# Performance work log

Measured on AMD Instinct MI355X. Metric: run time of the kernel, lower is better.

Reference implementation:

```python
import jax, jax.numpy as jnp
import numpy as np
from jax import lax

# Geometry constants (stand-in for beijing* globals)
A = 96           # beijingAngleNum
P = 4            # beijingPlanes
DET0, DET1 = 256, 8   # beijingSubDetectorSize [u, v]
NZ, NY, NX = 32, 256, 256  # beijingVolumeSize (nz = P * DET1)
T = 256          # ray integration steps
LAMB = 0.01


def _bilinear(vol, ix, iy):
    # vol: [nz, ny, nx]; ix, iy: [...] index-space coords. Zero outside.
    nz, ny, nx = vol.shape
    x0 = jnp.floor(ix); y0 = jnp.floor(iy)
    fx = (ix - x0).astype(vol.dtype); fy = (iy - y0).astype(vol.dtype)
    x0i = x0.astype(jnp.int32); y0i = y0.astype(jnp.int32)

    def g(yi, xi):
        valid = ((xi >= 0) & (xi < nx) & (yi >= 0) & (yi < ny)).astype(vol.dtype)
        v = vol[:, jnp.clip(yi, 0, ny - 1), jnp.clip(xi, 0, nx - 1)]  # [nz, ...]
        return v * valid

    return (g(y0i, x0i) * (1 - fy) * (1 - fx)
            + g(y0i, x0i + 1) * (1 - fy) * fx
            + g(y0i + 1, x0i) * fy * (1 - fx)
            + g(y0i + 1, x0i + 1) * fy * fx)


def forward_project(vol):
    # vol: [NZ, NY, NX] -> sinogram [A, NZ, DET0], parallel-beam over 180 deg
    angles = jnp.arange(A, dtype=jnp.float32) * (np.pi / A)
    u = jnp.arange(DET0, dtype=jnp.float32) - (DET0 - 1) / 2.0  # detector coord
    t = jnp.arange(T, dtype=jnp.float32) - (T - 1) / 2.0        # along-ray coord

    def per_angle(_, th):
        c, s = jnp.cos(th), jnp.sin(th)
        x = -u[:, None] * s + t[None, :] * c   # [DET0, T]
        y = u[:, None] * c + t[None, :] * s
        samp = _bilinear(vol, x + (NX - 1) / 2.0, y + (NY - 1) / 2.0)  # [NZ,DET0,T]
        return None, samp.sum(-1)  # line integral, [NZ, DET0]

    _, S = lax.scan(per_angle, None, angles)
    return S  # [A, NZ, DET0]


def back_project(S):
    # S: [A, NZ, DET0] -> volume [NZ, NY, NX] (adjoint-style backprojection)
    angles = jnp.arange(A, dtype=jnp.float32) * (np.pi / A)
    yy = jnp.arange(NY, dtype=jnp.float32) - (NY - 1) / 2.0
    xx = jnp.arange(NX, dtype=jnp.float32) - (NX - 1) / 2.0
    Y, X = jnp.meshgrid(yy, xx, indexing='ij')  # [NY, NX]

    def per_angle(acc, inp):
        th, Sa = inp  # Sa: [NZ, DET0]
        c, s = jnp.cos(th), jnp.sin(th)
        ub = -X * s + Y * c + (DET0 - 1) / 2.0  # detector bin coord [NY,NX]
        u0 = jnp.floor(ub)
        fu = (ub - u0).astype(Sa.dtype)
        u0i = u0.astype(jnp.int32)

        def g(ui):
            valid = ((ui >= 0) & (ui < DET0)).astype(Sa.dtype)
            return Sa[:, jnp.clip(ui, 0, DET0 - 1)] * valid  # [NZ,NY,NX]

        val = g(u0i) * (1 - fu) + g(u0i + 1) * fu
        return acc + val, None

    vol0 = jnp.zeros((NZ, NY, NX), dtype=S.dtype)
    vol, _ = lax.scan(per_angle, vol0, (angles, S))
    return vol


def setup_inputs() -> dict:
    key = jax.random.key(0)
    k1, k2 = jax.random.split(key)
    x = jax.random.normal(k1, (1, 1, NZ, NY, NX), dtype=jnp.float32)
    p = jax.random.normal(k2, (1, 1, A * P, DET1, DET0), dtype=jnp.float32)
    return {"x": x, "p": p}


def reference(x, p):
    vol = x[0, 0]                              # [NZ, NY, NX]
    S = forward_project(vol)                   # [A, NZ, DET0] native
    # ForwardProjection wrapper: (A,P,V,U) -> permute -> flat external layout
    ext = S.reshape(A, P, DET1, DET0).transpose(0, 2, 1, 3).reshape(1, 1, A * P, DET1, DET0)
    residual = ext - p
    # BackProjection wrapper: undo external layout back to native
    res_native = residual.reshape(A, DET1, P, DET0).transpose(0, 2, 1, 3).reshape(A, NZ, DET0)
    volb = back_project(res_native)            # [NZ, NY, NX]
    return (-LAMB * volb)[None, None]          # [1,1,NZ,NY,NX]
```

## Files before the change

### kernel.cpp

```cpp
#include <hip/hip_runtime.h>

#define A     96
#define DET0  256
#define NZ    32
#define NY    256
#define NX    256
#define T     256
#define LAMB  0.01f

#define TRIG_OFF  0
#define REST_OFF  256
#define VOLB_OFF  786688
#define PART_OFF  1835264
#define RES_ELEMS 786432

__device__ __forceinline__ unsigned short f2bf_rne(float f) {
    unsigned u = __float_as_uint(f);
    unsigned r = u + 0x7FFF + ((u >> 16) & 1);
    return (unsigned short)(r >> 16);
}
__device__ __forceinline__ float blo(unsigned u) { return __uint_as_float(u << 16); }
__device__ __forceinline__ float bhi(unsigned u) { return __uint_as_float(u & 0xFFFF0000u); }

__device__ __forceinline__ void acc8(float* acc, uint4 q, float w) {
    acc[0] = fmaf(w, blo(q.x), acc[0]); acc[1] = fmaf(w, bhi(q.x), acc[1]);
    acc[2] = fmaf(w, blo(q.y), acc[2]); acc[3] = fmaf(w, bhi(q.y), acc[3]);
    acc[4] = fmaf(w, blo(q.z), acc[4]); acc[5] = fmaf(w, bhi(q.z), acc[5]);
    acc[6] = fmaf(w, blo(q.w), acc[6]); acc[7] = fmaf(w, bhi(q.w), acc[7]);
}

__global__ __launch_bounds__(256) void k_transpose(const float* __restrict__ src,
                                                   unsigned short* __restrict__ vol_b,
                                                   float* __restrict__ trig) {
    __shared__ float lds[64 * 33];
    const int y   = blockIdx.y;
    const int x0  = blockIdx.x * 64;
    const int tid = threadIdx.x;

    if (blockIdx.x == 0 && y == 0 && tid < A) {
        float th = (float)tid * (float)(3.14159265358979323846 / (double)A);
        trig[2 * tid]     = cosf(th);
        trig[2 * tid + 1] = sinf(th);
    }

    const int xr = tid & 63;
    const int zr = tid >> 6;
    #pragma unroll
    for (int pz = 0; pz < 8; ++pz) {
        int z = pz * 4 + zr;
        lds[xr * 33 + z] = src[(z * NY + y) * NX + x0 + xr];
    }
    __syncthreads();
    const int zw = tid & 31;
    const int xw = tid >> 5;
    #pragma unroll
    for (int px = 0; px < 8; ++px) {
        int xi = px * 8 + xw;
        vol_b[(y * NX + x0 + xi) * NZ + zw] = f2bf_rne(lds[xi * 33 + zw]);
    }
}

__device__ __forceinline__ void rng(float g, float b, float L, float H,
                                    float& lo, float& hi) {
    if (fabsf(g) > 1e-5f) {
        float r0 = (L - b) / g, r1 = (H - b) / g;
        lo = fminf(r0, r1); hi = fmaxf(r0, r1);
    } else {
        bool in = (b >= L && b <= H);
        lo = in ? -1e9f : 1e9f;
        hi = in ? 1e9f : -1e9f;
    }
}
__device__ __forceinline__ int clampi(float v) {
    return (int)fminf(fmaxf(v, -2.f), 258.f);
}

__device__ __forceinline__ void sample_edge(const char* base, float ix, float iy,
                                            float* acc) {
    float xf = floorf(ix), yf = floorf(iy);
    float fx = ix - xf, fy = iy - yf;
    int x0 = (int)xf, y0 = (int)yf;
    float wx0 = 1.f - fx, wx1 = fx, wy0 = 1.f - fy, wy1 = fy;
    if ((unsigned)x0 >= NX)       wx0 = 0.f;
    if ((unsigned)(x0 + 1) >= NX) wx1 = 0.f;
    if ((unsigned)y0 >= NY)       wy0 = 0.f;
    if ((unsigned)(y0 + 1) >= NY) wy1 = 0.f;
    if ((wx0 == 0.f && wx1 == 0.f) || (wy0 == 0.f && wy1 == 0.f)) return;
    int cx0 = min(max(x0, 0), NX - 1);
    int cx1 = min(max(x0 + 1, 0), NX - 1);
    int cy0 = min(max(y0, 0), NY - 1);
    int cy1 = min(max(y0 + 1, 0), NY - 1);
    uint4 q00 = *(const uint4*)(base + ((size_t)((cy0 << 8) + cx0) << 6));
    uint4 q01 = *(const uint4*)(base + ((size_t)((cy0 << 8) + cx1) << 6));
    uint4 q10 = *(const uint4*)(base + ((size_t)((cy1 << 8) + cx0) << 6));
    uint4 q11 = *(const uint4*)(base + ((size_t)((cy1 << 8) + cx1) << 6));
    acc8(acc, q00, wy0 * wx0);
    acc8(acc, q01, wy0 * wx1);
    acc8(acc, q10, wy1 * wx0);
    acc8(acc, q11, wy1 * wx1);
}

__global__ __launch_bounds__(256) void k_forward(const unsigned short* __restrict__ vol_b,
                                                 const float* __restrict__ trig,
                                                 float* __restrict__ part,
                                                 int tlen) {
    const int tid = threadIdx.x;
    const int a  = blockIdx.z;
    const int u  = blockIdx.x * 64 + (tid >> 2);
    const int zq = tid & 3;
    const int t0 = blockIdx.y * tlen;

    const float c = trig[2 * a];
    const float s = trig[2 * a + 1];
    const float uu = (float)u - 127.5f;
    const float bx = fmaf(-uu, s, 127.5f);
    const float by = fmaf(uu, c, 127.5f);

    float lo1, hi1, lo2, hi2;
    rng(c, bx, -1.f, 256.f, lo1, hi1);
    rng(s, by, -1.f, 256.f, lo2, hi2);
    float fl = fmaxf(lo1, lo2), fh = fminf(hi1, hi2);
    int tF0 = max(t0, clampi(ceilf(fl + 127.5f)));
    int tF1 = min(t0 + tlen - 1, clampi(floorf(fh + 127.5f)));
    rng(c, bx, 1.f, 253.5f, lo1, hi1);
    rng(s, by, 1.f, 253.5f, lo2, hi2);
    float il = fmaxf(lo1, lo2), ih = fminf(hi1, hi2);
    int tI0 = max(clampi(ceilf(il + 127.5f)) + 1, tF0);
    int tI1 = min(clampi(floorf(ih + 127.5f)) - 1, tF1);
    if (tI0 > tI1) { tI0 = tF1 + 1; tI1 = tF1; }

    const char* base = (const char*)vol_b + zq * 16;
    float acc[8];
    #pragma unroll
    for (int k = 0; k < 8; ++k) acc[k] = 0.f;

    for (int t = tF0; t < tI0; ++t) {
        float ttf = (float)t - 127.5f;
        sample_edge(base, fmaf(ttf, c, bx), fmaf(ttf, s, by), acc);
    }
    for (int t = tI0; t <= tI1; ++t) {
        float ttf = (float)t - 127.5f;
        float ix = fmaf(ttf, c, bx);
        float iy = fmaf(ttf, s, by);
        float xf = floorf(ix), yf = floorf(iy);
        float fx = ix - xf, fy = iy - yf;
        int row = ((int)yf << 8) + (int)xf;
        const char* p0 = base + ((size_t)row << 6);
        uint4 q00 = *(const uint4*)(p0);
        uint4 q01 = *(const uint4*)(p0 + 64);
        uint4 q10 = *(const uint4*)(p0 + 16384);
        uint4 q11 = *(const uint4*)(p0 + 16384 + 64);
        float wx0 = 1.f - fx, wy0 = 1.f - fy;
        acc8(acc, q00, wy0 * wx0);
        acc8(acc, q01, wy0 * fx);
        acc8(acc, q10, fy * wx0);
        acc8(acc, q11, fy * fx);
    }
    for (int t = tI1 + 1; t <= tF1; ++t) {
        float ttf = (float)t - 127.5f;
        sample_edge(base, fmaf(ttf, c, bx), fmaf(ttf, s, by), acc);
    }

    float4* dst = (float4*)(part + (size_t)blockIdx.y * RES_ELEMS +
                            ((a * DET0 + u) * NZ + zq * 8));
    dst[0] = make_float4(acc[0], acc[1], acc[2], acc[3]);
    dst[1] = make_float4(acc[4], acc[5], acc[6], acc[7]);
}

__global__ __launch_bounds__(256) void k_combine(const float* __restrict__ p,
                                                 const float* __restrict__ part,
                                                 float* __restrict__ res_t,
                                                 int C) {
    __shared__ float lds[256 * 33];
    const int a = blockIdx.x;
    const int u = threadIdx.x;
    #pragma unroll
    for (int z = 0; z < 32; ++z) {
        int pidx = a * 8192 + (((z & 7) << 2) + (z >> 3)) * 256 + u;
        lds[u * 33 + z] = p[pidx];
    }
    __syncthreads();
    #pragma unroll
    for (int k = 0; k < 8; ++k) {
        int j4 = k * 256 + threadIdx.x;
        int j  = j4 * 4;
        int uu = j >> 5;
        int zb = j & 31;
        float4 v = make_float4(-lds[uu * 33 + zb],     -lds[uu * 33 + zb + 1],
                               -lds[uu * 33 + zb + 2], -lds[uu * 33 + zb + 3]);
        for (int c = 0; c < C; ++c) {
            float4 w = ((const float4*)(part + (size_t)c * RES_ELEMS))[a * 2048 + j4];
            v.x += w.x; v.y += w.y; v.z += w.z; v.w += w.w;
        }
        ((float4*)res_t)[a * 2048 + j4] = v;
    }
}

__global__ __launch_bounds__(256) void k_backward(const float* __restrict__ res_t,
                                                  const float* __restrict__ trig,
                                                  float* __restrict__ out) {
    __shared__ float4 wb[A * 32];
    __shared__ float  ob[32 * 33];
    const int tid = threadIdx.x;
    const int y  = blockIdx.y;
    const int xb = blockIdx.x * 32;

    for (int e = tid; e < A * 32; e += 256) {
        int a  = e >> 5;
        int xs = e & 31;
        float cc = trig[2 * a];
        float ss = trig[2 * a + 1];
        float xx = (float)(xb + xs) - 127.5f;
        float yy = (float)y - 127.5f;
        float ub = fmaf(-xx, ss, fmaf(yy, cc, 127.5f));
        float uf = floorf(ub);
        float fu = ub - uf;
        int i0 = (int)uf;
        float w0 = ((unsigned)i0 < DET0) ? (1.f - fu) : 0.f;
        float w1 = ((unsigned)(i0 + 1) < DET0) ? fu : 0.f;
        int c0 = min(max(i0, 0), DET0 - 1);
        int c1 = min(max(i0 + 1, 0), DET0 - 1);
        wb[e] = make_float4(w0, w1,
                            __int_as_float(((a * DET0 + c0) * NZ) << 2),
                            __int_as_float(((a * DET0 + c1) * NZ) << 2));
    }
    __syncthreads();

    const int xs = tid >> 3;
    const int zq = tid & 7;
    const char* rbase = (const char*)res_t + zq * 16;
    float4 acc = make_float4(0.f, 0.f, 0.f, 0.f);
    #pragma unroll 4
    for (int a = 0; a < A; ++a) {
        float4 e = wb[a * 32 + xs];
        float4 v0 = *(const float4*)(rbase + __float_as_int(e.z));
        float4 v1 = *(const float4*)(rbase + __float_as_int(e.w));
        acc.x = fmaf(e.x, v0.x, fmaf(e.y, v1.x, acc.x));
        acc.y = fmaf(e.x, v0.y, fmaf(e.y, v1.y, acc.y));
        acc.z = fmaf(e.x, v0.z, fmaf(e.y, v1.z, acc.z));
        acc.w = fmaf(e.x, v0.w, fmaf(e.y, v1.w, acc.w));
    }

    ob[(zq * 4 + 0) * 33 + xs] = acc.x;
    ob[(zq * 4 + 1) * 33 + xs] = acc.y;
    ob[(zq * 4 + 2) * 33 + xs] = acc.z;
    ob[(zq * 4 + 3) * 33 + xs] = acc.w;
    __syncthreads();

    const int z  = tid >> 3;
    const int x4 = (tid & 7) * 4;
    float4 o = make_float4(ob[z * 33 + x4],     ob[z * 33 + x4 + 1],
                           ob[z * 33 + x4 + 2], ob[z * 33 + x4 + 3]);
    float4* dst = (float4*)(out + (size_t)z * (NY * NX) + y * NX + xb + x4);
    *dst = make_float4(-LAMB * o.x, -LAMB * o.y, -LAMB * o.z, -LAMB * o.w);
}

extern "C" void kernel_launch(void* const* d_in, const int* in_sizes, int n_in,
                              void* d_out, int out_size, void* d_ws, size_t ws_size,
                              hipStream_t stream) {
    const float* x = (const float*)d_in[0];
    const float* p = (const float*)d_in[1];
    float* out = (float*)d_out;
    float* ws  = (float*)d_ws;

    float*          trig  = ws + TRIG_OFF;
    float*          res_t = ws + REST_OFF;
    unsigned short* vol_b = (unsigned short*)(ws + VOLB_OFF);
    float*          part  = ws + PART_OFF;

    size_t avail = ws_size / 4;
    int C = 8;
    while (C > 1 && (size_t)PART_OFF + (size_t)C * RES_ELEMS > avail) C >>= 1;
    int tlen = T / C;

    k_transpose<<<dim3(NX / 64, NY), 256, 0, stream>>>(x, vol_b, trig);
    k_forward  <<<dim3(4, C, A), 256, 0, stream>>>(vol_b, trig, part, tlen);
    k_combine  <<<dim3(A), 256, 0, stream>>>(p, part, res_t, C);
    k_backward <<<dim3(NX / 32, NY), 256, 0, stream>>>(res_t, trig, out);
}
```

Baseline: 205.8 us.

## Fuse residual init into transpose, atomically accumulate forward chunks, drop combine kernel

```diff
diff --git a/kernel.cpp b/kernel.cpp
--- a/kernel.cpp
+++ b/kernel.cpp
@@ -1,4 +1,5 @@
 #include <hip/hip_runtime.h>
+#include <hip/hip_fp16.h>
 
 #define A     96
 #define DET0  256
@@ -6,32 +7,31 @@
 #define NY    256
 #define NX    256
 #define T     256
+#define TLEN  32
+#define NCH   8
 #define LAMB  0.01f
 
 #define TRIG_OFF  0
 #define REST_OFF  256
 #define VOLB_OFF  786688
-#define PART_OFF  1835264
-#define RES_ELEMS 786432
-
-__device__ __forceinline__ unsigned short f2bf_rne(float f) {
-    unsigned u = __float_as_uint(f);
-    unsigned r = u + 0x7FFF + ((u >> 16) & 1);
-    return (unsigned short)(r >> 16);
-}
-__device__ __forceinline__ float blo(unsigned u) { return __uint_as_float(u << 16); }
-__device__ __forceinline__ float bhi(unsigned u) { return __uint_as_float(u & 0xFFFF0000u); }
-
-__device__ __forceinline__ void acc8(float* acc, uint4 q, float w) {
-    acc[0] = fmaf(w, blo(q.x), acc[0]); acc[1] = fmaf(w, bhi(q.x), acc[1]);
-    acc[2] = fmaf(w, blo(q.y), acc[2]); acc[3] = fmaf(w, bhi(q.y), acc[3]);
-    acc[4] = fmaf(w, blo(q.z), acc[4]); acc[5] = fmaf(w, bhi(q.z), acc[5]);
-    acc[6] = fmaf(w, blo(q.w), acc[6]); acc[7] = fmaf(w, bhi(q.w), acc[7]);
+
+__device__ __forceinline__ void accp(float* acc, unsigned v, float w) {
+    __half2 h = *reinterpret_cast<__half2*>(&v);
+    acc[0] = fmaf(w, __low2float(h),  acc[0]);
+    acc[1] = fmaf(w, __high2float(h), acc[1]);
+}
+__device__ __forceinline__ void acc8h(float* acc, uint4 q, float w) {
+    accp(acc + 0, q.x, w);
+    accp(acc + 2, q.y, w);
+    accp(acc + 4, q.z, w);
+    accp(acc + 6, q.w, w);
 }
 
 __global__ __launch_bounds__(256) void k_transpose(const float* __restrict__ src,
-                                                   unsigned short* __restrict__ vol_b,
-                                                   float* __restrict__ trig) {
+                                                   unsigned short* __restrict__ vol_h,
+                                                   float* __restrict__ trig,
+                                                   const float* __restrict__ p,
+                                                   float* __restrict__ res_t) {
     __shared__ float lds[64 * 33];
     const int y   = blockIdx.y;
     const int x0  = blockIdx.x * 64;
@@ -56,7 +56,34 @@
     #pragma unroll
     for (int px = 0; px < 8; ++px) {
         int xi = px * 8 + xw;
-        vol_b[(y * NX + x0 + xi) * NZ + zw] = f2bf_rne(lds[xi * 33 + zw]);
+        vol_h[(y * NX + x0 + xi) * NZ + zw] =
+            __half_as_ushort(__float2half(lds[xi * 33 + zw]));
+    }
+
+    if (y < A) {
+        const int a  = y;
+        const int u0 = blockIdx.x * 64;
+        __syncthreads();
+        const int col = tid & 63;
+        const int r0  = tid >> 6;
+        #pragma unroll
+        for (int i = 0; i < 8; ++i) {
+            int r = i * 4 + r0;
+            lds[r * 65 + col] = p[a * 8192 + r * 256 + u0 + col];
+        }
+        __syncthreads();
+        const int ul = tid >> 2;
+        const int zb = (tid & 3) * 8;
+        float o[8];
+        #pragma unroll
+        for (int k = 0; k < 8; ++k) {
+            int z = zb + k;
+            int r = ((z & 7) << 2) + (z >> 3);
+            o[k] = -lds[r * 65 + ul];
+        }
+        float4* d = (float4*)(res_t + (a * DET0 + u0 + ul) * NZ + zb);
+        d[0] = make_float4(o[0], o[1], o[2], o[3]);
+        d[1] = make_float4(o[4], o[5], o[6], o[7]);
     }
 }
 
@@ -94,21 +121,20 @@
     uint4 q01 = *(const uint4*)(base + ((size_t)((cy0 << 8) + cx1) << 6));
     uint4 q10 = *(const uint4*)(base + ((size_t)((cy1 << 8) + cx0) << 6));
     uint4 q11 = *(const uint4*)(base + ((size_t)((cy1 << 8) + cx1) << 6));
-    acc8(acc, q00, wy0 * wx0);
-    acc8(acc, q01, wy0 * wx1);
-    acc8(acc, q10, wy1 * wx0);
-    acc8(acc, q11, wy1 * wx1);
-}
-
-__global__ __launch_bounds__(256) void k_forward(const unsigned short* __restrict__ vol_b,
+    acc8h(acc, q00, wy0 * wx0);
+    acc8h(acc, q01, wy0 * wx1);
+    acc8h(acc, q10, wy1 * wx0);
+    acc8h(acc, q11, wy1 * wx1);
+}
+
+__global__ __launch_bounds__(256) void k_forward(const unsigned short* __restrict__ vol_h,
                                                  const float* __restrict__ trig,
-                                                 float* __restrict__ part,
-                                                 int tlen) {
+                                                 float* __restrict__ res_t) {
     const int tid = threadIdx.x;
     const int a  = blockIdx.z;
     const int u  = blockIdx.x * 64 + (tid >> 2);
     const int zq = tid & 3;
-    const int t0 = blockIdx.y * tlen;
+    const int t0 = blockIdx.y * TLEN;
 
     const float c = trig[2 * a];
     const float s = trig[2 * a + 1];
@@ -121,7 +147,8 @@
     rng(s, by, -1.f, 256.f, lo2, hi2);
     float fl = fmaxf(lo1, lo2), fh = fminf(hi1, hi2);
     int tF0 = max(t0, clampi(ceilf(fl + 127.5f)));
-    int tF1 = min(t0 + tlen - 1, clampi(floorf(fh + 127.5f)));
+    int tF1 = min(t0 + TLEN - 1, clampi(floorf(fh + 127.5f)));
+    if (tF1 < tF0) return;
     rng(c, bx, 1.f, 253.5f, lo1, hi1);
     rng(s, by, 1.f, 253.5f, lo2, hi2);
     float il = fmaxf(lo1, lo2), ih = fminf(hi1, hi2);
@@ -129,7 +156,7 @@
     int tI1 = min(clampi(floorf(ih + 127.5f)) - 1, tF1);
     if (tI0 > tI1) { tI0 = tF1 + 1; tI1 = tF1; }
 
-    const char* base = (const char*)vol_b + zq * 16;
+    const char* base = (const char*)vol_h + zq * 16;
     float acc[8];
     #pragma unroll
     for (int k = 0; k < 8; ++k) acc[k] = 0.f;
@@ -138,6 +165,7 @@
         float ttf = (float)t - 127.5f;
         sample_edge(base, fmaf(ttf, c, bx), fmaf(ttf, s, by), acc);
     }
+    #pragma unroll 2
     for (int t = tI0; t <= tI1; ++t) {
         float ttf = (float)t - 127.5f;
         float ix = fmaf(ttf, c, bx);
@@ -151,55 +179,26 @@
         uint4 q10 = *(const uint4*)(p0 + 16384);
         uint4 q11 = *(const uint4*)(p0 + 16384 + 64);
         float wx0 = 1.f - fx, wy0 = 1.f - fy;
-        acc8(acc, q00, wy0 * wx0);
-        acc8(acc, q01, wy0 * fx);
-        acc8(acc, q10, fy * wx0);
-        acc8(acc, q11, fy * fx);
+        acc8h(acc, q00, wy0 * wx0);
+        acc8h(acc, q01, wy0 * fx);
+        acc8h(acc, q10, fy * wx0);
+        acc8h(acc, q11, fy * fx);
     }
     for (int t = tI1 + 1; t <= tF1; ++t) {
         float ttf = (float)t - 127.5f;
         sample_edge(base, fmaf(ttf, c, bx), fmaf(ttf, s, by), acc);
     }
 
-    float4* dst = (float4*)(part + (size_t)blockIdx.y * RES_ELEMS +
-                            ((a * DET0 + u) * NZ + zq * 8));
-    dst[0] = make_float4(acc[0], acc[1], acc[2], acc[3]);
-    dst[1] = make_float4(acc[4], acc[5], acc[6], acc[7]);
-}
-
-__global__ __launch_bounds__(256) void k_combine(const float* __restrict__ p,
-                                                 const float* __restrict__ part,
-                                                 float* __restrict__ res_t,
-                                                 int C) {
-    __shared__ float lds[256 * 33];
-    const int a = blockIdx.x;
-    const int u = threadIdx.x;
-    #pragma unroll
-    for (int z = 0; z < 32; ++z) {
-        int pidx = a * 8192 + (((z & 7) << 2) + (z >> 3)) * 256 + u;
-        lds[u * 33 + z] = p[pidx];
-    }
-    __syncthreads();
-    #pragma unroll
-    for (int k = 0; k < 8; ++k) {
-        int j4 = k * 256 + threadIdx.x;
-        int j  = j4 * 4;
-        int uu = j >> 5;
-        int zb = j & 31;
-        float4 v = make_float4(-lds[uu * 33 + zb],     -lds[uu * 33 + zb + 1],
-                               -lds[uu * 33 + zb + 2], -lds[uu * 33 + zb + 3]);
-        for (int c = 0; c < C; ++c) {
-            float4 w = ((const float4*)(part + (size_t)c * RES_ELEMS))[a * 2048 + j4];
-            v.x += w.x; v.y += w.y; v.z += w.z; v.w += w.w;
-        }
-        ((float4*)res_t)[a * 2048 + j4] = v;
-    }
+    float* dst = res_t + ((a * DET0 + u) * NZ + zq * 8);
+    #pragma unroll
+    for (int k = 0; k < 8; ++k) unsafeAtomicAdd(dst + k, acc[k]);
 }
 
 __global__ __launch_bounds__(256) void k_backward(const float* __restrict__ res_t,
                                                   const float* __restrict__ trig,
                                                   float* __restrict__ out) {
-    __shared__ float4 wb[A * 32];
+    __shared__ float2 wbw[A * 32];
+    __shared__ int    wbo[A * 32];
     __shared__ float  ob[32 * 33];
     const int tid = threadIdx.x;
     const int y  = blockIdx.y;
@@ -218,11 +217,9 @@
         int i0 = (int)uf;
         float w0 = ((unsigned)i0 < DET0) ? (1.f - fu) : 0.f;
         float w1 = ((unsigned)(i0 + 1) < DET0) ? fu : 0.f;
-        int c0 = min(max(i0, 0), DET0 - 1);
-        int c1 = min(max(i0 + 1, 0), DET0 - 1);
-        wb[e] = make_float4(w0, w1,
-                            __int_as_float(((a * DET0 + c0) * NZ) << 2),
-                            __int_as_float(((a * DET0 + c1) * NZ) << 2));
+        int c1 = min(max(i0 + 1, 0), DET0);
+        wbw[e] = make_float2(w0, w1);
+        wbo[e] = ((a * DET0 + c1) * NZ - NZ) << 2;
     }
     __syncthreads();
 
@@ -232,13 +229,14 @@
     float4 acc = make_float4(0.f, 0.f, 0.f, 0.f);
     #pragma unroll 4
     for (int a = 0; a < A; ++a) {
-        float4 e = wb[a * 32 + xs];
-        float4 v0 = *(const float4*)(rbase + __float_as_int(e.z));
-        float4 v1 = *(const float4*)(rbase + __float_as_int(e.w));
-        acc.x = fmaf(e.x, v0.x, fmaf(e.y, v1.x, acc.x));
-        acc.y = fmaf(e.x, v0.y, fmaf(e.y, v1.y, acc.y));
-        acc.z = fmaf(e.x, v0.z, fmaf(e.y, v1.z, acc.z));
-        acc.w = fmaf(e.x, v0.w, fmaf(e.y, v1.w, acc.w));
+        float2 w  = wbw[a * 32 + xs];
+        int   off = wbo[a * 32 + xs];
+        float4 v0 = *(const float4*)(rbase + off);
+        float4 v1 = *(const float4*)(rbase + off + 128);
+        acc.x = fmaf(w.x, v0.x, fmaf(w.y, v1.x, acc.x));
+        acc.y = fmaf(w.x, v0.y, fmaf(w.y, v1.y, acc.y));
+        acc.z = fmaf(w.x, v0.z, fmaf(w.y, v1.z, acc.z));
+        acc.w = fmaf(w.x, v0.w, fmaf(w.y, v1.w, acc.w));
     }
 
     ob[(zq * 4 + 0) * 33 + xs] = acc.x;
@@ -265,16 +263,9 @@
 
     float*          trig  = ws + TRIG_OFF;
     float*          res_t = ws + REST_OFF;
-    unsigned short* vol_b = (unsigned short*)(ws + VOLB_OFF);
-    float*          part  = ws + PART_OFF;
-
-    size_t avail = ws_size / 4;
-    int C = 8;
-    while (C > 1 && (size_t)PART_OFF + (size_t)C * RES_ELEMS > avail) C >>= 1;
-    int tlen = T / C;
-
-    k_transpose<<<dim3(NX / 64, NY), 256, 0, stream>>>(x, vol_b, trig);
-    k_forward  <<<dim3(4, C, A), 256, 0, stream>>>(vol_b, trig, part, tlen);
-    k_combine  <<<dim3(A), 256, 0, stream>>>(p, part, res_t, C);
+    unsigned short* vol_h = (unsigned short*)(ws + VOLB_OFF);
+
+    k_transpose<<<dim3(NX / 64, NY), 256, 0, stream>>>(x, vol_h, trig, p, res_t);
+    k_forward  <<<dim3(4, NCH, A), 256, 0, stream>>>(vol_h, trig, res_t);
     k_backward <<<dim3(NX / 32, NY), 256, 0, stream>>>(res_t, trig, out);
 }
```

New measurement: 329.5 us. 1.6x slower.
